# Kernel optimization log

Hardware: AMD Instinct MI355X
Metric: run time of the kernel (lower is better)

The kernel has to match this reference:

```python
import jax, jax.numpy as jnp
import numpy as np

B, N, DIM, H, HD, COND, BS = 2, 1024, 768, 12, 64, 128, 16
S = 2 * N  # noised tokens [0:N) concatenated with clean x0 tokens [N:2N)
EPS = 1e-5
NEG = -1e30


def setup_inputs() -> dict:
    key = jax.random.key(0)
    ks = jax.random.split(key, 8)
    d = {}
    d['x'] = jax.random.normal(ks[0], (B, S, DIM), jnp.float32)
    d['c'] = jax.random.normal(ks[1], (B, COND), jnp.float32)
    # Rotary table for positions 0..N-1 (each half of the 2N sequence reuses the same positions)
    inv_freq = 1.0 / (10000.0 ** (np.arange(0, HD, 2, dtype=np.float64) / HD))
    freqs = np.arange(N, dtype=np.float64)[:, None] * inv_freq[None, :]
    emb = np.concatenate([freqs, freqs], axis=-1)  # [N, HD]
    cos = np.tile(np.cos(emb), (2, 1))[None, :, None, None, :]
    sin = np.tile(np.sin(emb), (2, 1))[None, :, None, None, :]
    d['cos'] = jnp.asarray(cos, jnp.float32)
    d['sin'] = jnp.asarray(sin, jnp.float32)
    # block-causal diffusion mask (flex_attention_mask): same (block, x0-flag) OR
    # cross-attention from noised block q>0 to strictly earlier CLEAN (x0) blocks
    idx = np.arange(S)
    fl = (idx >= N).astype(np.int64)
    blk = np.where(fl == 1, (idx - N) // BS, idx // BS)
    same = (blk[:, None] == blk[None, :]) & (fl[:, None] == fl[None, :])
    allowed = (blk[:, None] > 0) & (blk[None, :] < blk[:, None]) & (fl[None, :] == 1)
    d['mask'] = jnp.asarray(same | allowed)
    # parameters (adaLN is zero-init in the source; randomized here so the block is non-trivial)
    w = 0.02
    d['norm1_w'] = jnp.ones((DIM,), jnp.float32)
    d['qkv_w'] = jax.random.normal(ks[2], (3 * DIM, DIM), jnp.float32) * w
    d['attn_out_w'] = jax.random.normal(ks[3], (DIM, DIM), jnp.float32) * w
    d['norm2_w'] = jnp.ones((DIM,), jnp.float32)
    d['mlp_w1'] = jax.random.normal(ks[4], (4 * DIM, DIM), jnp.float32) * w
    d['mlp_b1'] = jnp.zeros((4 * DIM,), jnp.float32)
    d['mlp_w2'] = jax.random.normal(ks[5], (DIM, 4 * DIM), jnp.float32) * w
    d['mlp_b2'] = jnp.zeros((DIM,), jnp.float32)
    d['adaLN_w'] = jax.random.normal(ks[6], (6 * DIM, COND), jnp.float32) * w
    d['adaLN_b'] = jax.random.normal(ks[7], (6 * DIM,), jnp.float32) * w
    return d


def _ln(x, w):
    # F.layer_norm (no bias) followed by learned scale, as in the custom LayerNorm
    mu = x.mean(-1, keepdims=True)
    xc = x - mu
    var = (xc * xc).mean(-1, keepdims=True)
    return xc * jax.lax.rsqrt(var + EPS) * w


def reference(x, c, cos, sin, mask, norm1_w, qkv_w, attn_out_w, norm2_w,
              mlp_w1, mlp_b1, mlp_w2, mlp_b2, adaLN_w, adaLN_b):
    # adaLN modulation: [B, 6*DIM] -> six [B, 1, DIM] chunks
    mods = c @ adaLN_w.T + adaLN_b
    (shift_msa, scale_msa, gate_msa,
     shift_mlp, scale_mlp, gate_mlp) = jnp.split(mods[:, None, :], 6, axis=-1)
    x_skip = x
    h = _ln(x, norm1_w) * (1.0 + scale_msa) + shift_msa  # modulate_fused
    # qkv projection + rotary (torchscript path: qkv*cos + rotate_half(qkv)*sin)
    qkv = (h @ qkv_w.T).reshape(x.shape[0], S, 3, H, HD)
    rot = jnp.concatenate([-qkv[..., HD // 2:], qkv[..., :HD // 2]], axis=-1)
    qkv = qkv * cos + rot * sin
    q, k, v = qkv[:, :, 0], qkv[:, :, 1], qkv[:, :, 2]
    # SDPA with the block-causal diffusion mask, scale 1/sqrt(head_dim)
    scores = jnp.einsum('bqhd,bkhd->bhqk', q, k) / np.sqrt(HD).astype(np.float32)
    scores = jnp.where(mask[None, None], scores, NEG)
    p = jax.nn.softmax(scores, axis=-1)
    a = jnp.einsum('bhqk,bkhd->bqhd', p, v).reshape(x.shape[0], S, DIM)
    # bias_dropout_add_scale (inference => no dropout): gate * attn_out + residual
    x = gate_msa * (a @ attn_out_w.T) + x_skip
    h2 = _ln(x, norm2_w) * (1.0 + scale_mlp) + shift_mlp
    m = jax.nn.gelu(h2 @ mlp_w1.T + mlp_b1, approximate=True) @ mlp_w2.T + mlp_b2
    return x + gate_mlp * m
```

## Files before the change

### kernel.cpp

```cpp
#include <hip/hip_runtime.h>
#include <hip/hip_bf16.h>

#define EPS 1e-5f

typedef __attribute__((ext_vector_type(8))) short bf16x8;
typedef __attribute__((ext_vector_type(4))) short bf16x4;
typedef __attribute__((ext_vector_type(4))) float f32x4;

__device__ __forceinline__ f32x4 mfma_bf16(bf16x8 a, bf16x8 b, f32x4 c) {
    return __builtin_amdgcn_mfma_f32_16x16x32_bf16(a, b, c, 0, 0, 0);
}

__device__ __forceinline__ void async_ld16(const void* g, void* l) {
    __builtin_amdgcn_global_load_lds(
        (const __attribute__((address_space(1))) void*)g,
        (__attribute__((address_space(3))) void*)l, 16, 0, 0);
}

__device__ __forceinline__ float fast_gelu(float v) {
    float z2 = 1.5957691216057308f * (v + 0.044715f * v * v * v);
    float e = __expf(z2);
    return v * e / (e + 1.f);
}

__device__ __forceinline__ float bf2f(short s) {
    union { float f; unsigned u; } v;
    v.u = ((unsigned)(unsigned short)s) << 16;
    return v.f;
}

__global__ void k_pre(const float* __restrict__ a, __hip_bfloat16* __restrict__ oa, int na,
                      const float* __restrict__ b, __hip_bfloat16* __restrict__ ob, int nb,
                      const float* __restrict__ c, __hip_bfloat16* __restrict__ oc, int nc,
                      const float* __restrict__ d, __hip_bfloat16* __restrict__ od, int nd,
                      const float* __restrict__ cond, const float* __restrict__ alw,
                      const float* __restrict__ alb, float* __restrict__ mods) {
    if (blockIdx.x >= 27648) {
        int i = (blockIdx.x - 27648) * 256 + threadIdx.x;
        int bb = i / 4608, row = i - bb * 4608;
        const float4* cv = (const float4*)(cond + bb * 128);
        const float4* wv = (const float4*)(alw + (long)row * 128);
        float acc = 0.f;
#pragma unroll
        for (int k = 0; k < 32; ++k) {
            float4 x = cv[k], y = wv[k];
            acc += x.x * y.x + x.y * y.y + x.z * y.z + x.w * y.w;
        }
        mods[i] = acc + alb[row];
        return;
    }
    int i = blockIdx.x * 256 + threadIdx.x;
    if (i < na) { oa[i] = __float2bfloat16(a[i]); return; }
    i -= na;
    if (i < nb) { ob[i] = __float2bfloat16(b[i]); return; }
    i -= nb;
    if (i < nc) { oc[i] = __float2bfloat16(c[i]); return; }
    i -= nc;
    if (i < nd) od[i] = __float2bfloat16(d[i]);
}

__global__ void k_ln_mod(const float* __restrict__ x, const float* __restrict__ w,
                         const float* __restrict__ mods, int shiftOff, int scaleOff,
                         __hip_bfloat16* __restrict__ out) {
    int token = blockIdx.x;
    int lane = threadIdx.x;
    const float4* xr = (const float4*)(x + (long)token * 768);
    float4 v0 = xr[lane], v1 = xr[lane + 64], v2 = xr[lane + 128];
    float s  = v0.x + v0.y + v0.z + v0.w + v1.x + v1.y + v1.z + v1.w + v2.x + v2.y + v2.z + v2.w;
    float ss = v0.x*v0.x + v0.y*v0.y + v0.z*v0.z + v0.w*v0.w
             + v1.x*v1.x + v1.y*v1.y + v1.z*v1.z + v1.w*v1.w
             + v2.x*v2.x + v2.y*v2.y + v2.z*v2.z + v2.w*v2.w;
#pragma unroll
    for (int m = 32; m >= 1; m >>= 1) { s += __shfl_xor(s, m); ss += __shfl_xor(ss, m); }
    float mu = s * (1.f / 768.f);
    float var = ss * (1.f / 768.f) - mu * mu;
    float rs = rsqrtf(var + EPS);
    int b = token >> 11;
    const float* sh = mods + b * 4608 + shiftOff;
    const float* sc = mods + b * 4608 + scaleOff;
    __hip_bfloat16* o = out + (long)token * 768;
    float4 vv[3] = {v0, v1, v2};
#pragma unroll
    for (int kk = 0; kk < 3; ++kk) {
        int cbase = (lane + 64 * kk) * 4;
        const float* p = (const float*)&vv[kk];
#pragma unroll
        for (int j = 0; j < 4; ++j) {
            int col = cbase + j;
            float hv = (p[j] - mu) * rs * w[col] * (1.f + sc[col]) + sh[col];
            o[col] = __float2bfloat16(hv);
        }
    }
}

__global__ void k_red(const __hip_bfloat16* __restrict__ p, const float* __restrict__ x2,
                      const float* __restrict__ mods, const float* __restrict__ bias,
                      float* __restrict__ out) {
    long base = ((long)blockIdx.x * 256 + threadIdx.x) * 4;
    int col = (int)(base % 768);
    int row = (int)(base / 768);
    int b = row >> 11;
    short4 a0 = *(const short4*)(p + base);
    short4 a1 = *(const short4*)(p + 3145728 + base);
    float4 xr = *(const float4*)(x2 + base);
    float4 gt = *(const float4*)(mods + b * 4608 + 3840 + col);
    float4 bs = *(const float4*)(bias + col);
    float4 o;
    o.x = xr.x + gt.x * (bf2f(a0.x) + bf2f(a1.x) + bs.x);
    o.y = xr.y + gt.y * (bf2f(a0.y) + bf2f(a1.y) + bs.y);
    o.z = xr.z + gt.z * (bf2f(a0.z) + bf2f(a1.z) + bs.z);
    o.w = xr.w + gt.w * (bf2f(a0.w) + bf2f(a1.w) + bs.w);
    *(float4*)(out + base) = o;
}

__global__ __launch_bounds__(64) void k_attn(
    const __hip_bfloat16* __restrict__ q, const __hip_bfloat16* __restrict__ k,
    const __hip_bfloat16* __restrict__ vT, __hip_bfloat16* __restrict__ out) {
    __shared__ __hip_bfloat16 P[16 * 68];
    int lane = threadIdx.x;
    int l15 = lane & 15, quad = lane >> 4;
    int idx = blockIdx.x;
    int bh = idx % 24;
    int r = idx / 24;
    int fl, blk;
    if (r & 1) { fl = 1; blk = 63 - (r >> 1); }
    else       { fl = 0; blk = 63 - (r >> 1); }
    int qblk = fl * 64 + blk;

    const __hip_bfloat16* Q = q + ((long)bh * 2048 + qblk * 16) * 64;
    bf16x8 qa = *(const bf16x8*)(Q + l15 * 64 + quad * 8);
    bf16x8 qb = *(const bf16x8*)(Q + l15 * 64 + 32 + quad * 8);
    const __hip_bfloat16* K = k + (long)bh * 2048 * 64;
    const __hip_bfloat16* V = vT + (long)bh * 64 * 2048;

    const f32x4 vzero = {0.f, 0.f, 0.f, 0.f};
    f32x4 o[4]; float l[4];
#pragma unroll
    for (int rr = 0; rr < 4; ++rr) { o[rr] = vzero; l[rr] = 0.f; }

    int plen = (blk + fl) * 16;
    int pre = plen >> 4;
    int total16 = pre + (fl ? 0 : 1);
    int nIter = (total16 + 3) >> 2;

    auto stBase = [&](int t, bool act) -> int {
        return act ? ((t < pre) ? 1024 + t * 16 : blk * 16) : 0;
    };

    int st[4]; bool act[4];
    bf16x8 ka[4], kb8[4];
#pragma unroll
    for (int s = 0; s < 4; ++s) {
        act[s] = s < total16;
        st[s] = stBase(s, act[s]);
        const __hip_bfloat16* K0 = K + (long)st[s] * 64;
        ka[s]  = *(const bf16x8*)(K0 + l15 * 64 + quad * 8);
        kb8[s] = *(const bf16x8*)(K0 + l15 * 64 + 32 + quad * 8);
    }

    for (int ci = 0; ci < nIter; ++ci) {
        bf16x8 vf[2][4];
#pragma unroll
        for (int p2 = 0; p2 < 2; ++p2) {
            int kbv_lo = st[2 * p2], kbv_hi = st[2 * p2 + 1];
            int kbv = (quad < 2) ? kbv_lo : kbv_hi;
            int inner = (quad & 1) * 8;
#pragma unroll
            for (int tt = 0; tt < 4; ++tt)
                vf[p2][tt] = *(const bf16x8*)(V + (long)(tt * 16 + l15) * 2048 + kbv + inner);
        }

        f32x4 sc[4];
#pragma unroll
        for (int s = 0; s < 4; ++s)
            sc[s] = mfma_bf16(qb, kb8[s], mfma_bf16(qa, ka[s], vzero));

        int nst[4]; bool nact[4];
        bf16x8 nka[4], nkb[4];
        if (ci + 1 < nIter) {
#pragma unroll
            for (int s = 0; s < 4; ++s) {
                int t = 4 * (ci + 1) + s;
                nact[s] = t < total16;
                nst[s] = stBase(t, nact[s]);
                const __hip_bfloat16* K0 = K + (long)nst[s] * 64;
                nka[s] = *(const bf16x8*)(K0 + l15 * 64 + quad * 8);
                nkb[s] = *(const bf16x8*)(K0 + l15 * 64 + 32 + quad * 8);
            }
        }

#pragma unroll
        for (int s = 0; s < 4; ++s) {
#pragma unroll
            for (int rr = 0; rr < 4; ++rr) {
                float pv = act[s] ? __expf(sc[s][rr]) : 0.f;
                l[rr] += pv;
                P[(quad * 4 + rr) * 68 + s * 16 + l15] = __float2bfloat16(pv);
            }
        }
        asm volatile("s_waitcnt lgkmcnt(0)" ::: "memory");
        bf16x8 pa[2];
#pragma unroll
        for (int p2 = 0; p2 < 2; ++p2) {
            union { bf16x4 h[2]; bf16x8 v; } u;
            u.h[0] = *(const bf16x4*)(P + l15 * 68 + p2 * 32 + quad * 8);
            u.h[1] = *(const bf16x4*)(P + l15 * 68 + p2 * 32 + quad * 8 + 4);
            pa[p2] = u.v;
        }
        asm volatile("s_waitcnt lgkmcnt(0)" ::: "memory");
#pragma unroll
        for (int p2 = 0; p2 < 2; ++p2)
#pragma unroll
            for (int tt = 0; tt < 4; ++tt)
                o[tt] = mfma_bf16(pa[p2], vf[p2][tt], o[tt]);

        if (ci + 1 < nIter) {
#pragma unroll
            for (int s = 0; s < 4; ++s) {
                st[s] = nst[s]; act[s] = nact[s];
                ka[s] = nka[s]; kb8[s] = nkb[s];
            }
        }
    }

    int b = bh / 12, h = bh - b * 12;
    int seqbase = qblk * 16;
#pragma unroll
    for (int rr = 0; rr < 4; ++rr) {
        float lr = l[rr];
#pragma unroll
        for (int msk = 1; msk < 16; msk <<= 1) lr += __shfl_xor(lr, msk, 16);
        float inv = 1.f / lr;
        long row = b * 2048 + seqbase + quad * 4 + rr;
#pragma unroll
        for (int tt = 0; tt < 4; ++tt)
            out[row * 768 + h * 64 + tt * 16 + l15] = __float2bfloat16(o[tt][rr] * inv);
    }
}

template <int MODE, int TN>
__global__ __launch_bounds__(TN == 128 ? 256 : 128) void k_gemm(
    const __hip_bfloat16* __restrict__ A, const __hip_bfloat16* __restrict__ W,
    float* __restrict__ Cf, __hip_bfloat16* __restrict__ Cb,
    const float* __restrict__ bias, const float* __restrict__ mods, int gateOff,
    const float* __restrict__ resid, const float* __restrict__ cosb,
    const float* __restrict__ sinb, __hip_bfloat16* __restrict__ qo,
    __hip_bfloat16* __restrict__ ko, __hip_bfloat16* __restrict__ vo,
    int M, int N, int K, int lda) {
    constexpr int NW = (TN == 128) ? 4 : 2;
    constexpr int ACH = 512 / (NW * 64);
    constexpr int BCH = (TN * 4) / (NW * 64);
    constexpr int NINST = ACH + BCH;
    __shared__ __hip_bfloat16 lA[2][128 * 32];
    __shared__ __hip_bfloat16 lB[2][TN * 32];
    int t = threadIdx.x;
    int wave = t >> 6, lane = t & 63, l15 = lane & 15, quad = lane >> 4;
    int wr = (TN == 128) ? (wave >> 1) : wave;
    int wc = (TN == 128) ? (wave & 1) : 0;
    int sw8 = (quad ^ ((l15 >> 1) & 3)) * 8;
    long bm = blockIdx.x, bn = blockIdx.y;
    const __hip_bfloat16* Ab = A + bm * 128 * lda + (long)blockIdx.z * K;
    const __hip_bfloat16* Wb = W + bn * TN * lda + (long)blockIdx.z * K;

    long soffA[ACH], soffB[BCH];
#pragma unroll
    for (int cc = 0; cc < ACH; ++cc) {
        int chunk = cc * NW * 64 + t;
        int row = chunk >> 2;
        int c = (chunk & 3) ^ ((row >> 1) & 3);
        soffA[cc] = (long)row * lda + c * 8;
    }
#pragma unroll
    for (int cc = 0; cc < BCH; ++cc) {
        int chunk = cc * NW * 64 + t;
        int row = chunk >> 2;
        int c = (chunk & 3) ^ ((row >> 1) & 3);
        soffB[cc] = (long)row * lda + c * 8;
    }
    auto stage = [&](int k0, int buf) {
        char* lAc = (char*)&lA[buf][0];
        char* lBc = (char*)&lB[buf][0];
#pragma unroll
        for (int cc = 0; cc < ACH; ++cc)
            async_ld16(Ab + soffA[cc] + k0, lAc + cc * (NW * 1024) + wave * 1024);
#pragma unroll
        for (int cc = 0; cc < BCH; ++cc)
            async_ld16(Wb + soffB[cc] + k0, lBc + cc * (NW * 1024) + wave * 1024);
    };

    f32x4 acc[4][4];
#pragma unroll
    for (int i = 0; i < 4; ++i)
#pragma unroll
        for (int j = 0; j < 4; ++j) acc[i][j] = (f32x4){0.f, 0.f, 0.f, 0.f};

    int nIter = K / 32;
    stage(0, 0);
    for (int i = 0; i < nIter; ++i) {
        int cb = i & 1;
        if (i > 0) asm volatile("s_barrier" ::: "memory");
        if (i + 1 < nIter) {
            stage((i + 1) * 32, cb ^ 1);
            asm volatile("s_waitcnt vmcnt(%0)" :: "n"(NINST) : "memory");
        } else {
            asm volatile("s_waitcnt vmcnt(0)" ::: "memory");
        }
        asm volatile("s_barrier" ::: "memory");
        bf16x8 af[4], bfr[4];
#pragma unroll
        for (int ii = 0; ii < 4; ++ii)
            af[ii] = *(const bf16x8*)&lA[cb][(wr * 64 + ii * 16 + l15) * 32 + sw8];
#pragma unroll
        for (int j = 0; j < 4; ++j)
            bfr[j] = *(const bf16x8*)&lB[cb][(wc * 64 + j * 16 + l15) * 32 + sw8];
#pragma unroll
        for (int ii = 0; ii < 4; ++ii)
#pragma unroll
            for (int j = 0; j < 4; ++j)
                acc[ii][j] = mfma_bf16(af[ii], bfr[j], acc[ii][j]);
    }

    if (MODE == 4) {
        int hcol = (int)bn * 2 + wc;
        int th = hcol / 12, h = hcol % 12;
#pragma unroll
        for (int i = 0; i < 4; ++i) {
#pragma unroll
            for (int r = 0; r < 4; ++r) {
                int row = (int)bm * 128 + wr * 64 + i * 16 + quad * 4 + r;
                int s = row & 2047, b = row >> 11;
                long bh_ = b * 12 + h;
                const float* cbp = cosb + s * 64;
                const float* sbp = sinb + s * 64;
#pragma unroll
                for (int j = 0; j < 2; ++j) {
                    int dh = j * 16 + l15;
                    float a0f = acc[i][j][r], a1f = acc[i][j + 2][r];
                    float o0 = a0f * cbp[dh] - a1f * sbp[dh];
                    float o1 = a1f * cbp[dh + 32] + a0f * sbp[dh + 32];
                    if (th == 0) {
                        __hip_bfloat16* d = qo + (bh_ * 2048 + s) * 64;
                        d[dh]      = __float2bfloat16(o0 * 0.125f);
                        d[dh + 32] = __float2bfloat16(o1 * 0.125f);
                    } else if (th == 1) {
                        __hip_bfloat16* d = ko + (bh_ * 2048 + s) * 64;
                        d[dh]      = __float2bfloat16(o0);
                        d[dh + 32] = __float2bfloat16(o1);
                    } else {
                        __hip_bfloat16* d = vo + bh_ * 64 * 2048 + s;
                        d[(long)dh * 2048]        = __float2bfloat16(o0);
                        d[(long)(dh + 32) * 2048] = __float2bfloat16(o1);
                    }
                }
            }
        }
        return;
    }

#pragma unroll
    for (int i = 0; i < 4; ++i) {
#pragma unroll
        for (int j = 0; j < 4; ++j) {
#pragma unroll
            for (int r = 0; r < 4; ++r) {
                int row = (int)bm * 128 + wr * 64 + i * 16 + quad * 4 + r;
                int col = (int)bn * TN + wc * 64 + j * 16 + l15;
                float v = acc[i][j][r];
                long idx = (long)row * N + col;
                if (MODE == 1) {
                    Cf[idx] = mods[(row >> 11) * 4608 + gateOff + col] * v + resid[idx];
                } else if (MODE == 2) {
                    Cb[idx] = __float2bfloat16(fast_gelu(v + bias[col]));
                } else if (MODE == 3) {
                    Cf[idx] = resid[idx] + mods[(row >> 11) * 4608 + gateOff + col] * (v + bias[col]);
                } else {
                    Cb[(long)blockIdx.z * M * N + idx] = __float2bfloat16(v);
                }
            }
        }
    }
}

extern "C" void kernel_launch(void* const* d_in, const int* in_sizes, int n_in,
                              void* d_out, int out_size, void* d_ws, size_t ws_size,
                              hipStream_t stream) {
    const float* x    = (const float*)d_in[0];
    const float* c    = (const float*)d_in[1];
    const float* cosb = (const float*)d_in[2];
    const float* sinb = (const float*)d_in[3];
    const float* n1w  = (const float*)d_in[5];
    const float* qkvw = (const float*)d_in[6];
    const float* aow  = (const float*)d_in[7];
    const float* n2w  = (const float*)d_in[8];
    const float* w1   = (const float*)d_in[9];
    const float* b1   = (const float*)d_in[10];
    const float* w2   = (const float*)d_in[11];
    const float* b2   = (const float*)d_in[12];
    const float* alw  = (const float*)d_in[13];
    const float* alb  = (const float*)d_in[14];

    char* ws = (char*)d_ws;
    size_t off = 0;
    auto alloc = [&](size_t bytes) -> void* {
        void* p = ws + off;
        off += (bytes + 255) & ~(size_t)255;
        return p;
    };
    float*          mods = (float*)alloc(2 * 4608 * 4);
    __hip_bfloat16* hbuf = (__hip_bfloat16*)alloc((size_t)4096 * 768 * 2);
    __hip_bfloat16* qb   = (__hip_bfloat16*)alloc((size_t)24 * 2048 * 64 * 2);
    __hip_bfloat16* kb   = (__hip_bfloat16*)alloc((size_t)24 * 2048 * 64 * 2);
    __hip_bfloat16* vT   = (__hip_bfloat16*)alloc((size_t)24 * 64 * 2048 * 2);
    __hip_bfloat16* abuf = (__hip_bfloat16*)alloc((size_t)4096 * 768 * 2);
    float*          x2   = (float*)alloc((size_t)4096 * 768 * 4);
    __hip_bfloat16* h2   = (__hip_bfloat16*)alloc((size_t)4096 * 768 * 2);
    __hip_bfloat16* m1   = (__hip_bfloat16*)alloc((size_t)4096 * 3072 * 2);
    __hip_bfloat16* m2p  = (__hip_bfloat16*)alloc((size_t)2 * 4096 * 768 * 2);
    __hip_bfloat16* wq   = (__hip_bfloat16*)alloc((size_t)2304 * 768 * 2);
    __hip_bfloat16* wa   = (__hip_bfloat16*)alloc((size_t)768 * 768 * 2);
    __hip_bfloat16* w1b  = (__hip_bfloat16*)alloc((size_t)3072 * 768 * 2);
    __hip_bfloat16* w2b  = (__hip_bfloat16*)alloc((size_t)768 * 3072 * 2);

    k_pre<<<27684, 256, 0, stream>>>(qkvw, wq, 2304 * 768, aow, wa, 768 * 768,
                                     w1, w1b, 3072 * 768, w2, w2b, 768 * 3072,
                                     c, alw, alb, mods);
    k_ln_mod<<<4096, 64, 0, stream>>>(x, n1w, mods, 0, 768, hbuf);
    k_gemm<4, 128><<<dim3(32, 18), 256, 0, stream>>>(hbuf, wq, nullptr, nullptr, nullptr, nullptr, 0,
                                                     nullptr, cosb, sinb, qb, kb, vT,
                                                     4096, 2304, 768, 768);
    k_attn<<<3072, 64, 0, stream>>>(qb, kb, vT, abuf);
    k_gemm<1, 64><<<dim3(32, 12), 128, 0, stream>>>(abuf, wa, x2, nullptr, nullptr, mods, 1536,
                                                    x, nullptr, nullptr, nullptr, nullptr, nullptr,
                                                    4096, 768, 768, 768);
    k_ln_mod<<<4096, 64, 0, stream>>>(x2, n2w, mods, 2304, 3072, h2);
    k_gemm<2, 128><<<dim3(32, 24), 256, 0, stream>>>(h2, w1b, nullptr, m1, b1, nullptr, 0,
                                                     nullptr, nullptr, nullptr, nullptr, nullptr, nullptr,
                                                     4096, 3072, 768, 768);
    k_gemm<5, 128><<<dim3(32, 6, 2), 256, 0, stream>>>(m1, w2b, nullptr, m2p, nullptr, nullptr, 0,
                                                       nullptr, nullptr, nullptr, nullptr, nullptr, nullptr,
                                                       4096, 768, 1536, 3072);
    k_red<<<3072, 256, 0, stream>>>(m2p, x2, mods, b2, (float*)d_out);
}
```

Before: 316.1 us.

## Split attention key loop across four waves with LDS reduction

The attention kernel now launches 256 threads per block, and each of four wavefronts handles every fourth chunk of key blocks for the same 16-query tile. Partial outputs and row sums are written to shared memory, combined after a barrier, and each wave writes one 16-column slice of the output. This shortens the serial key loop for long-prefix query blocks, which should reduce tail latency. In exchange it adds LDS traffic, a sync, and idle waves for short rows where nIter is below four.

Result: slower. 341.1 us (+7.9%).

```diff
diff --git a/kernel.cpp b/kernel.cpp
--- a/kernel.cpp
+++ b/kernel.cpp
@@ -113,11 +113,15 @@
     *(float4*)(out + base) = o;
 }
 
-__global__ __launch_bounds__(64) void k_attn(
+__global__ __launch_bounds__(256, 4) void k_attn(
     const __hip_bfloat16* __restrict__ q, const __hip_bfloat16* __restrict__ k,
     const __hip_bfloat16* __restrict__ vT, __hip_bfloat16* __restrict__ out) {
-    __shared__ __hip_bfloat16 P[16 * 68];
-    int lane = threadIdx.x;
+    __shared__ __hip_bfloat16 P[4][16 * 68];
+    __shared__ float So[4][16][64];
+    __shared__ float Sl[4][4][64];
+    int tid = threadIdx.x;
+    int w = tid >> 6;
+    int lane = tid & 63;
     int l15 = lane & 15, quad = lane >> 4;
     int idx = blockIdx.x;
     int bh = idx % 24;
@@ -147,18 +151,23 @@
         return act ? ((t < pre) ? 1024 + t * 16 : blk * 16) : 0;
     };
 
+    __hip_bfloat16* Pw = &P[w][0];
+
     int st[4]; bool act[4];
     bf16x8 ka[4], kb8[4];
-#pragma unroll
-    for (int s = 0; s < 4; ++s) {
-        act[s] = s < total16;
-        st[s] = stBase(s, act[s]);
-        const __hip_bfloat16* K0 = K + (long)st[s] * 64;
-        ka[s]  = *(const bf16x8*)(K0 + l15 * 64 + quad * 8);
-        kb8[s] = *(const bf16x8*)(K0 + l15 * 64 + 32 + quad * 8);
-    }
-
-    for (int ci = 0; ci < nIter; ++ci) {
+    if (w < nIter) {
+#pragma unroll
+        for (int s = 0; s < 4; ++s) {
+            int t = 4 * w + s;
+            act[s] = t < total16;
+            st[s] = stBase(t, act[s]);
+            const __hip_bfloat16* K0 = K + (long)st[s] * 64;
+            ka[s]  = *(const bf16x8*)(K0 + l15 * 64 + quad * 8);
+            kb8[s] = *(const bf16x8*)(K0 + l15 * 64 + 32 + quad * 8);
+        }
+    }
+
+    for (int ci = w; ci < nIter; ci += 4) {
         bf16x8 vf[2][4];
 #pragma unroll
         for (int p2 = 0; p2 < 2; ++p2) {
@@ -177,10 +186,10 @@
 
         int nst[4]; bool nact[4];
         bf16x8 nka[4], nkb[4];
-        if (ci + 1 < nIter) {
+        if (ci + 4 < nIter) {
 #pragma unroll
             for (int s = 0; s < 4; ++s) {
-                int t = 4 * (ci + 1) + s;
+                int t = 4 * (ci + 4) + s;
                 nact[s] = t < total16;
                 nst[s] = stBase(t, nact[s]);
                 const __hip_bfloat16* K0 = K + (long)nst[s] * 64;
@@ -195,7 +204,7 @@
             for (int rr = 0; rr < 4; ++rr) {
                 float pv = act[s] ? __expf(sc[s][rr]) : 0.f;
                 l[rr] += pv;
-                P[(quad * 4 + rr) * 68 + s * 16 + l15] = __float2bfloat16(pv);
+                Pw[(quad * 4 + rr) * 68 + s * 16 + l15] = __float2bfloat16(pv);
             }
         }
         asm volatile("s_waitcnt lgkmcnt(0)" ::: "memory");
@@ -203,8 +212,8 @@
 #pragma unroll
         for (int p2 = 0; p2 < 2; ++p2) {
             union { bf16x4 h[2]; bf16x8 v; } u;
-            u.h[0] = *(const bf16x4*)(P + l15 * 68 + p2 * 32 + quad * 8);
-            u.h[1] = *(const bf16x4*)(P + l15 * 68 + p2 * 32 + quad * 8 + 4);
+            u.h[0] = *(const bf16x4*)(Pw + l15 * 68 + p2 * 32 + quad * 8);
+            u.h[1] = *(const bf16x4*)(Pw + l15 * 68 + p2 * 32 + quad * 8 + 4);
             pa[p2] = u.v;
         }
         asm volatile("s_waitcnt lgkmcnt(0)" ::: "memory");
@@ -214,7 +223,7 @@
             for (int tt = 0; tt < 4; ++tt)
                 o[tt] = mfma_bf16(pa[p2], vf[p2][tt], o[tt]);
 
-        if (ci + 1 < nIter) {
+        if (ci + 4 < nIter) {
 #pragma unroll
             for (int s = 0; s < 4; ++s) {
                 st[s] = nst[s]; act[s] = nact[s];
@@ -223,18 +232,27 @@
         }
     }
 
+#pragma unroll
+    for (int rr = 0; rr < 4; ++rr) {
+        float lr = l[rr];
+#pragma unroll
+        for (int msk = 1; msk < 16; msk <<= 1) lr += __shfl_xor(lr, msk, 16);
+        Sl[w][rr][lane] = lr;
+#pragma unroll
+        for (int tt = 0; tt < 4; ++tt) So[w][tt * 4 + rr][lane] = o[tt][rr];
+    }
+    __syncthreads();
+
     int b = bh / 12, h = bh - b * 12;
     int seqbase = qblk * 16;
 #pragma unroll
     for (int rr = 0; rr < 4; ++rr) {
-        float lr = l[rr];
-#pragma unroll
-        for (int msk = 1; msk < 16; msk <<= 1) lr += __shfl_xor(lr, msk, 16);
-        float inv = 1.f / lr;
+        float lsum = Sl[0][rr][lane] + Sl[1][rr][lane] + Sl[2][rr][lane] + Sl[3][rr][lane];
+        float ov = So[0][w * 4 + rr][lane] + So[1][w * 4 + rr][lane]
+                 + So[2][w * 4 + rr][lane] + So[3][w * 4 + rr][lane];
+        float inv = 1.f / lsum;
         long row = b * 2048 + seqbase + quad * 4 + rr;
-#pragma unroll
-        for (int tt = 0; tt < 4; ++tt)
-            out[row * 768 + h * 64 + tt * 16 + l15] = __float2bfloat16(o[tt][rr] * inv);
+        out[row * 768 + h * 64 + w * 16 + l15] = __float2bfloat16(ov * inv);
     }
 }
 
@@ -428,7 +446,7 @@
     k_gemm<4, 128><<<dim3(32, 18), 256, 0, stream>>>(hbuf, wq, nullptr, nullptr, nullptr, nullptr, 0,
                                                      nullptr, cosb, sinb, qb, kb, vT,
                                                      4096, 2304, 768, 768);
-    k_attn<<<3072, 64, 0, stream>>>(qb, kb, vT, abuf);
+    k_attn<<<3072, 256, 0, stream>>>(qb, kb, vT, abuf);
     k_gemm<1, 64><<<dim3(32, 12), 128, 0, stream>>>(abuf, wa, x2, nullptr, nullptr, mods, 1536,
                                                     x, nullptr, nullptr, nullptr, nullptr, nullptr,
                                                     4096, 768, 768, 768);
```

## Share K/V tiles across four query blocks via double-buffered LDS in attention

Applied to the files above, without the earlier changes.

The attention kernel now launches 256-thread workgroups in which four waves handle two adjacent block indices for both the noised and clean halves. Because these query blocks attend to nearly the same clean-prefix keys, K and V tiles are staged once into swizzled, double-buffered LDS with async global-to-LDS loads, and per-wave activity masks select which key tiles each wave uses. This is meant to cut redundant global K/V traffic and overlap the next tile's loads with compute. The cost is workgroup barriers, extra LDS use, and some masked wasted work for waves whose key range is shorter.

New measurement: 291.7 us. 1.08x faster.

```diff
diff --git a/kernel.cpp b/kernel.cpp
--- a/kernel.cpp
+++ b/kernel.cpp
@@ -113,18 +113,19 @@
     *(float4*)(out + base) = o;
 }
 
-__global__ __launch_bounds__(64) void k_attn(
+__global__ __launch_bounds__(256) void k_attn(
     const __hip_bfloat16* __restrict__ q, const __hip_bfloat16* __restrict__ k,
     const __hip_bfloat16* __restrict__ vT, __hip_bfloat16* __restrict__ out) {
-    __shared__ __hip_bfloat16 P[16 * 68];
-    int lane = threadIdx.x;
-    int l15 = lane & 15, quad = lane >> 4;
+    __shared__ __hip_bfloat16 KL[2][64 * 64];
+    __shared__ __hip_bfloat16 VL[2][64 * 64];
+    __shared__ __hip_bfloat16 P[4][16 * 68];
+    int tid = threadIdx.x;
+    int w = tid >> 6, lane = tid & 63, l15 = lane & 15, quad = lane >> 4;
     int idx = blockIdx.x;
     int bh = idx % 24;
-    int r = idx / 24;
-    int fl, blk;
-    if (r & 1) { fl = 1; blk = 63 - (r >> 1); }
-    else       { fl = 0; blk = 63 - (r >> 1); }
+    int gi = idx / 24;
+    int b0 = 62 - 2 * gi;
+    int fl = w & 1, blk = b0 + (w >> 1);
     int qblk = fl * 64 + blk;
 
     const __hip_bfloat16* Q = q + ((long)bh * 2048 + qblk * 16) * 64;
@@ -133,69 +134,106 @@
     const __hip_bfloat16* K = k + (long)bh * 2048 * 64;
     const __hip_bfloat16* V = vT + (long)bh * 64 * 2048;
 
+    auto kbase = [&](int t) -> int {
+        if (t < b0 + 2) return 1024 + t * 16;
+        if (t == b0 + 2) return b0 * 16;
+        if (t == b0 + 3) return (b0 + 1) * 16;
+        return 0;
+    };
+    auto active = [&](int t) -> bool {
+        if (w == 0) return t < b0 || t == b0 + 2;
+        if (w == 1) return t < b0 + 1;
+        if (w == 2) return t < b0 + 1 || t == b0 + 3;
+        return t < b0 + 2;
+    };
+
+    int kkr[2], kbs[2], vsi[2], vki[2];
+#pragma unroll
+    for (int i = 0; i < 2; ++i) {
+        int o = i * 4096 + tid * 16;
+        kkr[i] = o >> 7;
+        int b = o & 127;
+        kbs[i] = b ^ ((kkr[i] & 7) << 4);
+        int lk2 = b ^ ((kkr[i] & 7) << 4);
+        vsi[i] = lk2 >> 5;
+        vki[i] = (lk2 & 31) >> 1;
+    }
+    auto stage = [&](int ci, int buf) {
+#pragma unroll
+        for (int i = 0; i < 2; ++i) {
+            int gk = kbase(4 * ci + (kkr[i] >> 4)) + (kkr[i] & 15);
+            async_ld16(K + (long)gk * 64 + (kbs[i] >> 1),
+                       (char*)&KL[buf][0] + i * 4096 + tid * 16);
+        }
+#pragma unroll
+        for (int i = 0; i < 2; ++i) {
+            int gk = kbase(4 * ci + vsi[i]) + vki[i];
+            async_ld16(V + (long)kkr[i] * 2048 + gk,
+                       (char*)&VL[buf][0] + i * 4096 + tid * 16);
+        }
+    };
+
+    int kfo[4][2], vfo[2][4];
+#pragma unroll
+    for (int s = 0; s < 4; ++s)
+#pragma unroll
+        for (int h = 0; h < 2; ++h)
+            kfo[s][h] = (s * 16 + l15) * 64 +
+                        (((h * 64 + quad * 16) ^ ((l15 & 7) << 4)) >> 1);
+#pragma unroll
+    for (int p2 = 0; p2 < 2; ++p2)
+#pragma unroll
+        for (int tt = 0; tt < 4; ++tt) {
+            int d = tt * 16 + l15;
+            int c = (p2 * 64 + (quad >> 1) * 32 + (quad & 1) * 16) ^ ((l15 & 7) << 4);
+            vfo[p2][tt] = d * 64 + (c >> 1);
+        }
+
     const f32x4 vzero = {0.f, 0.f, 0.f, 0.f};
     f32x4 o[4]; float l[4];
 #pragma unroll
     for (int rr = 0; rr < 4; ++rr) { o[rr] = vzero; l[rr] = 0.f; }
 
-    int plen = (blk + fl) * 16;
-    int pre = plen >> 4;
-    int total16 = pre + (fl ? 0 : 1);
-    int nIter = (total16 + 3) >> 2;
-
-    auto stBase = [&](int t, bool act) -> int {
-        return act ? ((t < pre) ? 1024 + t * 16 : blk * 16) : 0;
-    };
-
-    int st[4]; bool act[4];
-    bf16x8 ka[4], kb8[4];
-#pragma unroll
-    for (int s = 0; s < 4; ++s) {
-        act[s] = s < total16;
-        st[s] = stBase(s, act[s]);
-        const __hip_bfloat16* K0 = K + (long)st[s] * 64;
-        ka[s]  = *(const bf16x8*)(K0 + l15 * 64 + quad * 8);
-        kb8[s] = *(const bf16x8*)(K0 + l15 * 64 + 32 + quad * 8);
-    }
-
+    int nIter = (b0 + 7) >> 2;
+    __hip_bfloat16* Pw = &P[w][0];
+
+    stage(0, 0);
     for (int ci = 0; ci < nIter; ++ci) {
-        bf16x8 vf[2][4];
-#pragma unroll
-        for (int p2 = 0; p2 < 2; ++p2) {
-            int kbv_lo = st[2 * p2], kbv_hi = st[2 * p2 + 1];
-            int kbv = (quad < 2) ? kbv_lo : kbv_hi;
-            int inner = (quad & 1) * 8;
-#pragma unroll
-            for (int tt = 0; tt < 4; ++tt)
-                vf[p2][tt] = *(const bf16x8*)(V + (long)(tt * 16 + l15) * 2048 + kbv + inner);
-        }
-
+        int cb = ci & 1;
+        if (ci > 0) asm volatile("s_barrier" ::: "memory");
+        if (ci + 1 < nIter) {
+            stage(ci + 1, cb ^ 1);
+            asm volatile("s_waitcnt vmcnt(4)" ::: "memory");
+        } else {
+            asm volatile("s_waitcnt vmcnt(0)" ::: "memory");
+        }
+        asm volatile("s_barrier" ::: "memory");
+
+        bf16x8 ka[4], kb8[4];
+#pragma unroll
+        for (int s = 0; s < 4; ++s) {
+            ka[s]  = *(const bf16x8*)&KL[cb][kfo[s][0]];
+            kb8[s] = *(const bf16x8*)&KL[cb][kfo[s][1]];
+        }
         f32x4 sc[4];
 #pragma unroll
         for (int s = 0; s < 4; ++s)
             sc[s] = mfma_bf16(qb, kb8[s], mfma_bf16(qa, ka[s], vzero));
-
-        int nst[4]; bool nact[4];
-        bf16x8 nka[4], nkb[4];
-        if (ci + 1 < nIter) {
-#pragma unroll
-            for (int s = 0; s < 4; ++s) {
-                int t = 4 * (ci + 1) + s;
-                nact[s] = t < total16;
-                nst[s] = stBase(t, nact[s]);
-                const __hip_bfloat16* K0 = K + (long)nst[s] * 64;
-                nka[s] = *(const bf16x8*)(K0 + l15 * 64 + quad * 8);
-                nkb[s] = *(const bf16x8*)(K0 + l15 * 64 + 32 + quad * 8);
-            }
-        }
+        bf16x8 vf[2][4];
+#pragma unroll
+        for (int p2 = 0; p2 < 2; ++p2)
+#pragma unroll
+            for (int tt = 0; tt < 4; ++tt)
+                vf[p2][tt] = *(const bf16x8*)&VL[cb][vfo[p2][tt]];
 
 #pragma unroll
         for (int s = 0; s < 4; ++s) {
+            bool a = active(4 * ci + s);
 #pragma unroll
             for (int rr = 0; rr < 4; ++rr) {
-                float pv = act[s] ? __expf(sc[s][rr]) : 0.f;
+                float pv = a ? __expf(sc[s][rr]) : 0.f;
                 l[rr] += pv;
-                P[(quad * 4 + rr) * 68 + s * 16 + l15] = __float2bfloat16(pv);
+                Pw[(quad * 4 + rr) * 68 + s * 16 + l15] = __float2bfloat16(pv);
             }
         }
         asm volatile("s_waitcnt lgkmcnt(0)" ::: "memory");
@@ -203,8 +241,8 @@
 #pragma unroll
         for (int p2 = 0; p2 < 2; ++p2) {
             union { bf16x4 h[2]; bf16x8 v; } u;
-            u.h[0] = *(const bf16x4*)(P + l15 * 68 + p2 * 32 + quad * 8);
-            u.h[1] = *(const bf16x4*)(P + l15 * 68 + p2 * 32 + quad * 8 + 4);
+            u.h[0] = *(const bf16x4*)(Pw + l15 * 68 + p2 * 32 + quad * 8);
+            u.h[1] = *(const bf16x4*)(Pw + l15 * 68 + p2 * 32 + quad * 8 + 4);
             pa[p2] = u.v;
         }
         asm volatile("s_waitcnt lgkmcnt(0)" ::: "memory");
@@ -213,14 +251,6 @@
 #pragma unroll
             for (int tt = 0; tt < 4; ++tt)
                 o[tt] = mfma_bf16(pa[p2], vf[p2][tt], o[tt]);
-
-        if (ci + 1 < nIter) {
-#pragma unroll
-            for (int s = 0; s < 4; ++s) {
-                st[s] = nst[s]; act[s] = nact[s];
-                ka[s] = nka[s]; kb8[s] = nkb[s];
-            }
-        }
     }
 
     int b = bh / 12, h = bh - b * 12;
@@ -428,7 +458,7 @@
     k_gemm<4, 128><<<dim3(32, 18), 256, 0, stream>>>(hbuf, wq, nullptr, nullptr, nullptr, nullptr, 0,
                                                      nullptr, cosb, sinb, qb, kb, vT,
                                                      4096, 2304, 768, 768);
-    k_attn<<<3072, 64, 0, stream>>>(qb, kb, vT, abuf);
+    k_attn<<<768, 256, 0, stream>>>(qb, kb, vT, abuf);
     k_gemm<1, 64><<<dim3(32, 12), 128, 0, stream>>>(abuf, wa, x2, nullptr, nullptr, mods, 1536,
                                                     x, nullptr, nullptr, nullptr, nullptr, nullptr,
                                                     4096, 768, 768, 768);
```
